# Kernel optimization log

Hardware: AMD Instinct MI355X
Metric: run time of the kernel (lower is better)

The kernel has to match this reference:

```python
import jax, jax.numpy as jnp
import numpy as np

SS, D, V = 64, 256, 10000
B, S = 16, 512


def setup_inputs() -> dict:
    key = jax.random.key(0)
    ks = jax.random.split(key, 7)
    scale = lambda fan_in: 1.0 / np.sqrt(fan_in)
    return {
        "x": jax.random.normal(ks[0], (B, S, D), dtype=jnp.float32),
        # nn.Linear(D, 4*ss): weight [4ss, D], bias [4ss]
        "Wxs_w": jax.random.uniform(ks[1], (4 * SS, D), jnp.float32, -scale(D), scale(D)),
        "Wxs_b": jax.random.uniform(ks[2], (4 * SS,), jnp.float32, -scale(D), scale(D)),
        # nn.Linear(ss, 4*ss)
        "Wss_w": jax.random.uniform(ks[3], (4 * SS, SS), jnp.float32, -scale(SS), scale(SS)),
        "Wss_b": jax.random.uniform(ks[4], (4 * SS,), jnp.float32, -scale(SS), scale(SS)),
        # nn.Linear(ss, V)
        "Wsy_w": jax.random.uniform(ks[5], (V, SS), jnp.float32, -scale(SS), scale(SS)),
        "Wsy_b": jax.random.uniform(ks[6], (V,), jnp.float32, -scale(SS), scale(SS)),
    }


def reference(x, Wxs_w, Wxs_b, Wss_w, Wss_b, Wsy_w, Wsy_b):
    b, s, _ = x.shape
    ss = Wss_w.shape[1]
    # Precompute input projections for all timesteps: [s, b, 4ss]
    xproj = jnp.einsum("bsd,kd->sbk", x, Wxs_w) + Wxs_b

    def step(carry, xp_t):
        h, c = carry
        comb = xp_t + h @ Wss_w.T + Wss_b  # [b, 4ss]
        f, i, g, o = jnp.split(comb, 4, axis=-1)
        f = jax.nn.sigmoid(f)
        i = jax.nn.sigmoid(i)
        o = jax.nn.sigmoid(o)
        g = jnp.tanh(g)
        c = c * f + i * g
        h = o * c  # NOTE: original code omits tanh(c) here; stay faithful
        return (h, c), h

    h0 = jnp.zeros((b, ss), dtype=x.dtype)
    c0 = jnp.zeros((b, ss), dtype=x.dtype)
    _, hs = jax.lax.scan(step, (h0, c0), xproj)  # hs: [s, b, ss]
    # Per-step vocab projection == batched projection of stacked hidden states
    y = jnp.einsum("sbh,vh->bsv", hs, Wsy_w) + Wsy_b  # [b, s, V]
    return y
```

## Files before the change

### kernel.cpp

```cpp
#include <hip/hip_runtime.h>

typedef unsigned short u16;
typedef unsigned int u32;

using short8 = __attribute__((ext_vector_type(8))) short;
using f32x4  = __attribute__((ext_vector_type(4))) float;
using f32x2  = __attribute__((ext_vector_type(2))) float;

#define SSEQ 512
#define BB   16
#define DD   256
#define G4   256
#define SSZ  64
#define VV   10000
#define VPAD 10112
#define MALL 8192

#define OFF_XHI   0u
#define OFF_XLO   4194304u
#define OFF_WHI   8388608u
#define OFF_WLO   8519680u
#define OFF_WSY   8650752u
#define OFF_XPROJ 9945088u
#define OFF_HS    18333696u

__device__ __forceinline__ u16 f2bf(float f) {
  u32 u = __float_as_uint(f);
  u32 r = (u + 0x7fffu + ((u >> 16) & 1u)) >> 16;
  return (u16)r;
}
__device__ __forceinline__ float bf2f(u16 h) {
  return __uint_as_float(((u32)h) << 16);
}
__device__ __forceinline__ f32x2 pkfma(f32x2 a, f32x2 b, f32x2 c) {
  asm("v_pk_fma_f32 %0, %1, %2, %0" : "+v"(c) : "v"(a), "v"(b));
  return c;
}

#define NX 2097152
#define NW 65536
#define NP 647168
__global__ void k0_convert(const float* __restrict__ x, const float* __restrict__ Wxs,
                           const float* __restrict__ Wsy,
                           u16* __restrict__ xhi, u16* __restrict__ xlo,
                           u16* __restrict__ whi, u16* __restrict__ wlo,
                           u16* __restrict__ wsyb) {
  int i = blockIdx.x * 256 + threadIdx.x;
  if (i < NX) {
    float v = x[i]; u16 h = f2bf(v);
    xhi[i] = h; xlo[i] = f2bf(v - bf2f(h));
  } else if (i < NX + NW) {
    int j = i - NX;
    float v = Wxs[j]; u16 h = f2bf(v);
    whi[j] = h; wlo[j] = f2bf(v - bf2f(h));
  } else if (i < NX + NW + NP) {
    int j = i - NX - NW;
    wsyb[j] = (j < VV * SSZ) ? f2bf(Wsy[j]) : (u16)0;
  }
}

__global__ __launch_bounds__(256) void k1_xproj(
    const u16* __restrict__ xhi, const u16* __restrict__ xlo,
    const u16* __restrict__ whi, const u16* __restrict__ wlo,
    const float* __restrict__ bias, float* __restrict__ xproj) {
  int bid = blockIdx.x;
  int mb = bid >> 1, nb = bid & 1;
  int tid = threadIdx.x, l = tid & 63, wid = tid >> 6;
  int wm = wid >> 1, wv = wid & 1;
  int m0 = mb * 128 + wm * 64, n0 = nb * 128 + wv * 64;
  int lr = l & 15, lg = l >> 4;

  f32x4 acc[4][4];
#pragma unroll
  for (int a = 0; a < 4; a++)
#pragma unroll
    for (int bq = 0; bq < 4; bq++) acc[a][bq] = (f32x4){0.f, 0.f, 0.f, 0.f};

#pragma unroll
  for (int p = 0; p < 3; p++) {
    const u16* A = (p == 1) ? xlo : xhi;
    const u16* B = (p == 2) ? wlo : whi;
#pragma unroll
    for (int ks = 0; ks < 8; ks++) {
      short8 af[4], bf_[4];
#pragma unroll
      for (int fm = 0; fm < 4; fm++)
        af[fm] = *(const short8*)(A + (size_t)(m0 + fm * 16 + lr) * 256 + ks * 32 + lg * 8);
#pragma unroll
      for (int fv = 0; fv < 4; fv++)
        bf_[fv] = *(const short8*)(B + (size_t)(n0 + fv * 16 + lr) * 256 + ks * 32 + lg * 8);
#pragma unroll
      for (int fm = 0; fm < 4; fm++)
#pragma unroll
        for (int fv = 0; fv < 4; fv++)
          acc[fm][fv] = __builtin_amdgcn_mfma_f32_16x16x32_bf16(af[fm], bf_[fv], acc[fm][fv], 0, 0, 0);
    }
  }
#pragma unroll
  for (int fv = 0; fv < 4; fv++) {
    int j = n0 + fv * 16 + lr;
    float bj = bias[j];
#pragma unroll
    for (int fm = 0; fm < 4; fm++)
#pragma unroll
      for (int r = 0; r < 4; r++) {
        int m = m0 + fm * 16 + lg * 4 + r;
        xproj[(size_t)m * 256 + j] = acc[fm][fv][r] + bj;
      }
  }
}

__global__ __launch_bounds__(256, 1) void k2_scan(
    const float* __restrict__ xproj, const float* __restrict__ Wss,
    const float* __restrict__ Wssb, u16* __restrict__ hsb) {
  __shared__ float hbuf[2][64];
  __shared__ u16 hstage[SSEQ][64];

  int b = blockIdx.x, tid = threadIdx.x;
  int w = tid >> 6, l = tid & 63;
  int s = l & 15, g = l >> 4;
  int jj = w * 16 + s;
  int row = g * 64 + jj;

  f32x2 wr[32];
  const f32x2* pw = (const f32x2*)(Wss + (size_t)row * 64);
#pragma unroll
  for (int q = 0; q < 32; q++) wr[q] = pw[q];
  float bg = Wssb[row];

  float kk = (g == 2) ? 2.885390082f : -1.442695041f;
  float Ac = (g == 2) ? 1.f : 0.f;
  float Bc = (g == 2) ? -2.f : 1.f;

  f32x4 h4[16];
#pragma unroll
  for (int q = 0; q < 16; q++) h4[q] = (f32x4){0.f, 0.f, 0.f, 0.f};
  float c = 0.f;

  const float* xpb = xproj + (size_t)b * SSEQ * 256 + row;
  float xp0 = xpb[0];
  float xp1 = xpb[256];

  for (int t = 0; t < SSEQ; t++) {
    float xp2 = (t + 2 < SSEQ) ? xpb[(size_t)(t + 2) * 256] : 0.f;

    f32x2 a0 = (f32x2){bg + xp0, 0.f};
    f32x2 a1 = (f32x2){0.f, 0.f};
    f32x2 a2 = (f32x2){0.f, 0.f};
    f32x2 a3 = (f32x2){0.f, 0.f};
#pragma unroll
    for (int q = 0; q < 8; q++) {
      f32x2 hA0 = (f32x2){h4[2 * q][0], h4[2 * q][1]};
      f32x2 hB0 = (f32x2){h4[2 * q][2], h4[2 * q][3]};
      f32x2 hA1 = (f32x2){h4[2 * q + 1][0], h4[2 * q + 1][1]};
      f32x2 hB1 = (f32x2){h4[2 * q + 1][2], h4[2 * q + 1][3]};
      a0 = pkfma(hA0, wr[4 * q + 0], a0);
      a1 = pkfma(hB0, wr[4 * q + 1], a1);
      a2 = pkfma(hA1, wr[4 * q + 2], a2);
      a3 = pkfma(hB1, wr[4 * q + 3], a3);
    }
    float a = ((a0[0] + a0[1]) + (a1[0] + a1[1])) + ((a2[0] + a2[1]) + (a3[0] + a3[1]));

    float z = exp2f(kk * a);
    float act = fmaf(Bc, __builtin_amdgcn_rcpf(z + 1.f), Ac);

    float fg = __shfl(act, s, 64);
    float ig = __shfl(act, 16 + s, 64);
    float gg = __shfl(act, 32 + s, 64);
    float og = __shfl(act, 48 + s, 64);

    c = fmaf(c, fg, ig * gg);
    float hn = og * c;

    if (g == 0) {
      hbuf[t & 1][jj] = hn;
      hstage[t][jj] = f2bf(hn);
    }
    asm volatile("s_waitcnt lgkmcnt(0)\n\ts_barrier" ::: "memory");

    const f32x4* hb = (const f32x4*)hbuf[t & 1];
#pragma unroll
    for (int q = 0; q < 16; q++) h4[q] = hb[q];

    xp0 = xp1; xp1 = xp2;
  }

  __syncthreads();
  const uint4* src = (const uint4*)hstage;
  uint4* dst = (uint4*)(hsb + (size_t)b * SSEQ * 64);
#pragma unroll
  for (int i = 0; i < 16; i++) dst[tid + 256 * i] = src[tid + 256 * i];
}

__global__ __launch_bounds__(256) void k3_y(
    const u16* __restrict__ hsb, const u16* __restrict__ wsyb,
    const float* __restrict__ bias, float* __restrict__ y) {
  int bid = blockIdx.x;
  int mb = bid / 79, vb = bid - mb * 79;
  int tid = threadIdx.x, l = tid & 63, wid = tid >> 6;
  int wm = wid >> 1, wv = wid & 1;
  int m0 = mb * 128 + wm * 64, v0 = vb * 128 + wv * 64;
  int lr = l & 15, lg = l >> 4;

  f32x4 acc[4][4];
#pragma unroll
  for (int a = 0; a < 4; a++)
#pragma unroll
    for (int bq = 0; bq < 4; bq++) acc[a][bq] = (f32x4){0.f, 0.f, 0.f, 0.f};

#pragma unroll
  for (int ks = 0; ks < 2; ks++) {
    short8 af[4], bf_[4];
#pragma unroll
    for (int fm = 0; fm < 4; fm++)
      af[fm] = *(const short8*)(hsb + (size_t)(m0 + fm * 16 + lr) * 64 + ks * 32 + lg * 8);
#pragma unroll
    for (int fv = 0; fv < 4; fv++)
      bf_[fv] = *(const short8*)(wsyb + (size_t)(v0 + fv * 16 + lr) * 64 + ks * 32 + lg * 8);
#pragma unroll
    for (int fv = 0; fv < 4; fv++)
#pragma unroll
      for (int fm = 0; fm < 4; fm++)
        acc[fv][fm] = __builtin_amdgcn_mfma_f32_16x16x32_bf16(bf_[fv], af[fm], acc[fv][fm], 0, 0, 0);
  }

#pragma unroll
  for (int fv = 0; fv < 4; fv++) {
    int vb4 = v0 + fv * 16 + lg * 4;
    bool ok = (vb4 + 3) < VV;
    float4 bv = ok ? *(const float4*)(bias + vb4) : float4{0.f, 0.f, 0.f, 0.f};
#pragma unroll
    for (int fm = 0; fm < 4; fm++) {
      int m = m0 + fm * 16 + lr;
      if (ok) {
        float4 o;
        o.x = acc[fv][fm][0] + bv.x;
        o.y = acc[fv][fm][1] + bv.y;
        o.z = acc[fv][fm][2] + bv.z;
        o.w = acc[fv][fm][3] + bv.w;
        *(float4*)(y + (size_t)m * (size_t)VV + vb4) = o;
      }
    }
  }
}

extern "C" void kernel_launch(void* const* d_in, const int* in_sizes, int n_in,
                              void* d_out, int out_size, void* d_ws, size_t ws_size,
                              hipStream_t stream) {
  const float* x     = (const float*)d_in[0];
  const float* Wxs_w = (const float*)d_in[1];
  const float* Wxs_b = (const float*)d_in[2];
  const float* Wss_w = (const float*)d_in[3];
  const float* Wss_b = (const float*)d_in[4];
  const float* Wsy_w = (const float*)d_in[5];
  const float* Wsy_b = (const float*)d_in[6];
  float* y = (float*)d_out;
  char* ws = (char*)d_ws;

  u16*   xhi   = (u16*)(ws + OFF_XHI);
  u16*   xlo   = (u16*)(ws + OFF_XLO);
  u16*   whi   = (u16*)(ws + OFF_WHI);
  u16*   wlo   = (u16*)(ws + OFF_WLO);
  u16*   wsyb  = (u16*)(ws + OFF_WSY);
  float* xproj = (float*)(ws + OFF_XPROJ);
  u16*   hsb   = (u16*)(ws + OFF_HS);

  k0_convert<<<(NX + NW + NP) / 256, 256, 0, stream>>>(x, Wxs_w, Wsy_w, xhi, xlo, whi, wlo, wsyb);
  k1_xproj<<<128, 256, 0, stream>>>(xhi, xlo, whi, wlo, Wxs_b, xproj);
  k2_scan<<<16, 256, 0, stream>>>(xproj, Wss_w, Wss_b, hsb);
  k3_y<<<64 * 79, 256, 0, stream>>>(hsb, wsyb, Wsy_b, y);
}
```

Before: 328.4 us.

## Split LSTM recurrence dot products across lanes with DPP reduction

Reorganizes the scan kernel so each group of 4 lanes owns one hidden unit and splits the 64-wide recurrent dot product into four 16-element slices, one per lane, for all four gates. Partial sums are combined with DPP quad adds instead of four cross-lane shuffles per step. Each lane now reads only 16 hidden values from LDS per step instead of 64, and every lane computes all four gate activations redundantly. This shortens the serial per-step critical path of LDS reads, FMAs and shuffles, at the cost of extra transcendental work and the DPP reduction.

```diff
diff --git a/kernel.cpp b/kernel.cpp
--- a/kernel.cpp
+++ b/kernel.cpp
@@ -35,6 +35,11 @@
 __device__ __forceinline__ f32x2 pkfma(f32x2 a, f32x2 b, f32x2 c) {
   asm("v_pk_fma_f32 %0, %1, %2, %0" : "+v"(c) : "v"(a), "v"(b));
   return c;
+}
+template <int CTRL>
+__device__ __forceinline__ float qadd(float x) {
+  int pv = __builtin_amdgcn_update_dpp(0, __float_as_int(x), CTRL, 0xf, 0xf, true);
+  return x + __int_as_float(pv);
 }
 
 #define NX 2097152
@@ -118,71 +123,79 @@
 
   int b = blockIdx.x, tid = threadIdx.x;
   int w = tid >> 6, l = tid & 63;
-  int s = l & 15, g = l >> 4;
-  int jj = w * 16 + s;
-  int row = g * 64 + jj;
+  int oo = l >> 2, ks = l & 3;
+  int jj = w * 16 + oo;
 
   f32x2 wr[32];
-  const f32x2* pw = (const f32x2*)(Wss + (size_t)row * 64);
-#pragma unroll
-  for (int q = 0; q < 32; q++) wr[q] = pw[q];
-  float bg = Wssb[row];
-
-  float kk = (g == 2) ? 2.885390082f : -1.442695041f;
-  float Ac = (g == 2) ? 1.f : 0.f;
-  float Bc = (g == 2) ? -2.f : 1.f;
-
-  f32x4 h4[16];
-#pragma unroll
-  for (int q = 0; q < 16; q++) h4[q] = (f32x4){0.f, 0.f, 0.f, 0.f};
+  float bias4[4];
+#pragma unroll
+  for (int g = 0; g < 4; g++) {
+    const f32x2* pw = (const f32x2*)(Wss + (size_t)(g * 64 + jj) * 64 + ks * 16);
+#pragma unroll
+    for (int q = 0; q < 8; q++) wr[g * 8 + q] = pw[q];
+    bias4[g] = Wssb[g * 64 + jj];
+  }
+
+  const float* xpb = xproj + (size_t)b * SSEQ * 256 + jj;
+  float xpc[4], xpn[4];
+#pragma unroll
+  for (int g = 0; g < 4; g++) xpc[g] = xpb[g * 64];
+
+  if (tid < 128) ((float*)hbuf)[tid] = 0.f;
+  __syncthreads();
+
   float c = 0.f;
 
-  const float* xpb = xproj + (size_t)b * SSEQ * 256 + row;
-  float xp0 = xpb[0];
-  float xp1 = xpb[256];
-
   for (int t = 0; t < SSEQ; t++) {
-    float xp2 = (t + 2 < SSEQ) ? xpb[(size_t)(t + 2) * 256] : 0.f;
-
-    f32x2 a0 = (f32x2){bg + xp0, 0.f};
-    f32x2 a1 = (f32x2){0.f, 0.f};
-    f32x2 a2 = (f32x2){0.f, 0.f};
-    f32x2 a3 = (f32x2){0.f, 0.f};
-#pragma unroll
-    for (int q = 0; q < 8; q++) {
-      f32x2 hA0 = (f32x2){h4[2 * q][0], h4[2 * q][1]};
-      f32x2 hB0 = (f32x2){h4[2 * q][2], h4[2 * q][3]};
-      f32x2 hA1 = (f32x2){h4[2 * q + 1][0], h4[2 * q + 1][1]};
-      f32x2 hB1 = (f32x2){h4[2 * q + 1][2], h4[2 * q + 1][3]};
-      a0 = pkfma(hA0, wr[4 * q + 0], a0);
-      a1 = pkfma(hB0, wr[4 * q + 1], a1);
-      a2 = pkfma(hA1, wr[4 * q + 2], a2);
-      a3 = pkfma(hB1, wr[4 * q + 3], a3);
-    }
-    float a = ((a0[0] + a0[1]) + (a1[0] + a1[1])) + ((a2[0] + a2[1]) + (a3[0] + a3[1]));
-
-    float z = exp2f(kk * a);
-    float act = fmaf(Bc, __builtin_amdgcn_rcpf(z + 1.f), Ac);
-
-    float fg = __shfl(act, s, 64);
-    float ig = __shfl(act, 16 + s, 64);
-    float gg = __shfl(act, 32 + s, 64);
-    float og = __shfl(act, 48 + s, 64);
+    int rb = (t + 1) & 1;
+    f32x4 h4[4];
+    const f32x4* hb = (const f32x4*)&hbuf[rb][ks * 16];
+    h4[0] = hb[0]; h4[1] = hb[1]; h4[2] = hb[2]; h4[3] = hb[3];
+
+    if (t + 1 < SSEQ) {
+      const float* xn = xpb + (size_t)(t + 1) * 256;
+#pragma unroll
+      for (int g = 0; g < 4; g++) xpn[g] = xn[g * 64];
+    }
+
+    float p[4];
+#pragma unroll
+    for (int g = 0; g < 4; g++) {
+      f32x2 a0 = (f32x2){0.f, 0.f}, a1 = (f32x2){0.f, 0.f};
+#pragma unroll
+      for (int q = 0; q < 4; q++) {
+        f32x2 hA = (f32x2){h4[q][0], h4[q][1]};
+        f32x2 hB = (f32x2){h4[q][2], h4[q][3]};
+        a0 = pkfma(hA, wr[g * 8 + 2 * q], a0);
+        a1 = pkfma(hB, wr[g * 8 + 2 * q + 1], a1);
+      }
+      p[g] = (a0[0] + a0[1]) + (a1[0] + a1[1]);
+    }
+
+#pragma unroll
+    for (int g = 0; g < 4; g++) p[g] = qadd<0x4E>(qadd<0xB1>(p[g]));
+
+    float pf = p[0] + xpc[0] + bias4[0];
+    float pi = p[1] + xpc[1] + bias4[1];
+    float pg = p[2] + xpc[2] + bias4[2];
+    float po = p[3] + xpc[3] + bias4[3];
+
+    float fg = __builtin_amdgcn_rcpf(1.f + exp2f(-1.442695041f * pf));
+    float ig = __builtin_amdgcn_rcpf(1.f + exp2f(-1.442695041f * pi));
+    float og = __builtin_amdgcn_rcpf(1.f + exp2f(-1.442695041f * po));
+    float gg = fmaf(-2.f, __builtin_amdgcn_rcpf(exp2f(2.885390082f * pg) + 1.f), 1.f);
 
     c = fmaf(c, fg, ig * gg);
     float hn = og * c;
 
-    if (g == 0) {
+    if (ks == 0) {
       hbuf[t & 1][jj] = hn;
       hstage[t][jj] = f2bf(hn);
     }
     asm volatile("s_waitcnt lgkmcnt(0)\n\ts_barrier" ::: "memory");
 
-    const f32x4* hb = (const f32x4*)hbuf[t & 1];
-#pragma unroll
-    for (int q = 0; q < 16; q++) h4[q] = hb[q];
-
-    xp0 = xp1; xp1 = xp2;
+#pragma unroll
+    for (int g = 0; g < 4; g++) xpc[g] = xpn[g];
   }
 
   __syncthreads();
```

Result: faster. 315.5 us (-3.9%).
